# Performance work log

Hardware: AMD Instinct MI355X
Metric: run time of the kernel (lower is better)

The kernel has to match this reference:

```python
import jax, jax.numpy as jnp
import numpy as np

B, SV, SA, D, H, L, F = 1, 2048, 512, 1024, 16, 2, 4096
DH = D // H
S = SV + SA


def layer_norm(x):
    mu = jnp.mean(x, axis=-1, keepdims=True)
    var = jnp.var(x, axis=-1, keepdims=True)
    return (x - mu) * jax.lax.rsqrt(var + 1e-6)


def rms_norm(x, g):
    return x * jax.lax.rsqrt(jnp.mean(x * x, axis=-1, keepdims=True) + 1e-6) * g


def rope(x, theta):
    # x: [B,S,H*DH], theta: [S, DH//2] angles; complex-pair rotation as in rope_apply
    b, s, _ = x.shape
    x4 = x.reshape(b, s, H, DH)
    xe, xo = x4[..., 0::2], x4[..., 1::2]
    c = jnp.cos(theta)[None, :, None, :]
    sn = jnp.sin(theta)[None, :, None, :]
    re = xe * c - xo * sn
    im = xe * sn + xo * c
    return jnp.stack([re, im], axis=-1).reshape(b, s, H * DH)


def setup_inputs() -> dict:
    key = jax.random.key(0)
    ks = jax.random.split(key, 20)
    w = 0.02
    inp = {
        'video_tokens': jax.random.normal(ks[0], (B, SV, D), jnp.float32),
        'action_tokens': jax.random.normal(ks[1], (B, SA, D), jnp.float32),
        'video_freqs': jax.random.uniform(ks[2], (SV, DH // 2), jnp.float32) * 6.28,
        'action_freqs': jax.random.uniform(ks[3], (SA, DH // 2), jnp.float32) * 6.28,
        'video_t_mod': jax.random.normal(ks[4], (B, 6, D), jnp.float32),
        'action_t_mod': jax.random.normal(ks[5], (B, 6, D), jnp.float32),
        'Wq': jax.random.normal(ks[6], (2, L, D, D), jnp.float32) * w,
        'Wk': jax.random.normal(ks[7], (2, L, D, D), jnp.float32) * w,
        'Wv': jax.random.normal(ks[8], (2, L, D, D), jnp.float32) * w,
        'Wo': jax.random.normal(ks[9], (2, L, D, D), jnp.float32) * w,
        'bq': jnp.zeros((2, L, D), jnp.float32),
        'bk': jnp.zeros((2, L, D), jnp.float32),
        'bv': jnp.zeros((2, L, D), jnp.float32),
        'bo': jnp.zeros((2, L, D), jnp.float32),
        'gq': jnp.ones((2, L, D), jnp.float32),
        'gk': jnp.ones((2, L, D), jnp.float32),
        'mod': jax.random.normal(ks[10], (2, L, 6, D), jnp.float32) * 0.02,
        'W1': jax.random.normal(ks[11], (2, L, D, F), jnp.float32) * w,
        'b1': jnp.zeros((2, L, F), jnp.float32),
        'W2': jax.random.normal(ks[12], (2, L, F, D), jnp.float32) * w,
        'b2': jnp.zeros((2, L, D), jnp.float32),
    }
    # Mixed-modality ctx_mask: video bidirectional; action attends video + causal over action
    m = np.zeros((S, S), dtype=bool)
    m[:SV, :SV] = True
    m[SV:, :SV] = True
    m[SV:, SV:] = np.tril(np.ones((SA, SA), dtype=bool))
    inp['attention_mask'] = jnp.asarray(m)
    return inp


def _mot_forward(video_tokens, action_tokens, video_freqs, action_freqs,
                 video_t_mod, action_t_mod, Wq, Wk, Wv, Wo, bq, bk, bv, bo,
                 gq, gk, mod, W1, b1, W2, b2, attention_mask):
    xs = [video_tokens, action_tokens]
    thetas = [video_freqs, action_freqs]
    tmods = [video_t_mod, action_t_mod]
    scale = 1.0 / jnp.sqrt(jnp.asarray(DH, xs[0].dtype))
    for l in range(L):
        qs, kss, vs, posts = [], [], [], []
        for e in range(2):
            m6 = mod[e, l][None] + tmods[e]  # [B,6,D]
            sh_msa, sc_msa, g_msa, sh_mlp, sc_mlp, g_mlp = (
                m6[:, i:i + 1, :] for i in range(6))
            a = layer_norm(xs[e]) * (1.0 + sc_msa) + sh_msa
            q = rope(rms_norm(a @ Wq[e, l] + bq[e, l], gq[e, l]), thetas[e])
            k = rope(rms_norm(a @ Wk[e, l] + bk[e, l], gk[e, l]), thetas[e])
            v = a @ Wv[e, l] + bv[e, l]
            qs.append(q); kss.append(k); vs.append(v)
            posts.append((g_msa, sh_mlp, sc_mlp, g_mlp))
        qc = jnp.concatenate(qs, axis=1).reshape(B, S, H, DH)
        kc = jnp.concatenate(kss, axis=1).reshape(B, S, H, DH)
        vc = jnp.concatenate(vs, axis=1).reshape(B, S, H, DH)
        scores = jnp.einsum('bqhd,bkhd->bhqk', qc, kc) * scale
        scores = jnp.where(attention_mask[None, None], scores, -1e9)
        p = jax.nn.softmax(scores, axis=-1)
        o = jnp.einsum('bhqk,bkhd->bqhd', p, vc).reshape(B, S, H * DH)
        outs = [o[:, :SV], o[:, SV:]]
        for e in range(2):
            g_msa, sh_mlp, sc_mlp, g_mlp = posts[e]
            x = xs[e] + g_msa * (outs[e] @ Wo[e, l] + bo[e, l])
            mi = layer_norm(x) * (1.0 + sc_mlp) + sh_mlp
            h = jax.nn.gelu(mi @ W1[e, l] + b1[e, l], approximate=True) @ W2[e, l] + b2[e, l]
            xs[e] = x + g_mlp * h
    return jnp.concatenate(xs, axis=1)  # [B, SV+SA, D]


def reference(video_tokens, action_tokens, video_freqs, action_freqs,
              video_t_mod, action_t_mod, Wq, Wk, Wv, Wo, bq, bk, bv, bo,
              gq, gk, mod, W1, b1, W2, b2, attention_mask):
    return _mot_forward(video_tokens, action_tokens, video_freqs, action_freqs,
                        video_t_mod, action_t_mod, Wq, Wk, Wv, Wo, bq, bk, bv, bo,
                        gq, gk, mod, W1, b1, W2, b2, attention_mask)
```

## Files before the change

kernel.cpp:

```cpp
#include <hip/hip_runtime.h>
#include <hip/hip_bf16.h>

#define BF16 __hip_bfloat16
typedef short bf16x8 __attribute__((ext_vector_type(8)));
typedef float f32x4  __attribute__((ext_vector_type(4)));
typedef unsigned int u32;

#define MFMA16(a, b, c) __builtin_amdgcn_mfma_f32_16x16x32_bf16(a, b, c, 0, 0, 0)


__device__ __forceinline__ void async16(const void* g, void* l) {
  __builtin_amdgcn_global_load_lds(
      (const __attribute__((address_space(1))) u32*)g,
      (__attribute__((address_space(3))) u32*)l, 16, 0, 0);
}

__device__ __forceinline__ u32 pkbf(float a, float b) {
  union { BF16 h; unsigned short s; } ua, ub;
  ua.h = __float2bfloat16(a); ub.h = __float2bfloat16(b);
  return (u32)ua.s | ((u32)ub.s << 16);
}

__global__ __launch_bounds__(256) void wtrans(const float* __restrict__ W,
                                              BF16* __restrict__ WT, int K, int N,
                                              size_t outZ) {
  __shared__ float t[32][33];
  const float* Wm = W + (size_t)K * N * blockIdx.z;
  BF16* Tm = WT + outZ * blockIdx.z;
  int n0 = blockIdx.x * 32, k0 = blockIdx.y * 32;
  int tx = threadIdx.x & 31, ty = threadIdx.x >> 5;
#pragma unroll
  for (int i = 0; i < 4; i++)
    t[ty + 8 * i][tx] = Wm[(size_t)(k0 + ty + 8 * i) * N + n0 + tx];
  __syncthreads();
#pragma unroll
  for (int i = 0; i < 4; i++)
    Tm[(size_t)(n0 + ty + 8 * i) * K + k0 + tx] = __float2bfloat16(t[tx][ty + 8 * i]);
}

__global__ __launch_bounds__(256) void packb(const float* __restrict__ bq,
                                             const float* __restrict__ bk,
                                             const float* __restrict__ bv,
                                             float* __restrict__ bqkv) {
  int i = blockIdx.x * 256 + threadIdx.x;
  int s = i / 3072, c = i - s * 3072;
  float v = (c < 1024) ? bq[s * 1024 + c]
          : (c < 2048) ? bk[s * 1024 + c - 1024]
                       : bv[s * 1024 + c - 2048];
  bqkv[i] = v;
}

__global__ __launch_bounds__(256) void ln_mod(const float* __restrict__ x,
                                              BF16* __restrict__ out,
                                              const float* __restrict__ mod,
                                              const float* __restrict__ tmv,
                                              const float* __restrict__ tma,
                                              int l, int ish, int isc) {
  int r = blockIdx.x;
  int e = (r >= 2048) ? 1 : 0;
  const float* tm = e ? tma : tmv;
  const float* mo = mod + (size_t)((e * 2 + l) * 6) * 1024;
  float4 v = ((const float4*)(x + (size_t)r * 1024))[threadIdx.x];
  float s = v.x + v.y + v.z + v.w;
  float s2 = v.x * v.x + v.y * v.y + v.z * v.z + v.w * v.w;
#pragma unroll
  for (int off = 32; off >= 1; off >>= 1) {
    s += __shfl_down(s, off);
    s2 += __shfl_down(s2, off);
  }
  __shared__ float red[8];
  int lane = threadIdx.x & 63, w = threadIdx.x >> 6;
  if (lane == 0) { red[w] = s; red[4 + w] = s2; }
  __syncthreads();
  s = red[0] + red[1] + red[2] + red[3];
  s2 = red[4] + red[5] + red[6] + red[7];
  float mu = s * (1.f / 1024.f);
  float var = s2 * (1.f / 1024.f) - mu * mu;
  float inv = rsqrtf(var + 1e-6f);
  int c = threadIdx.x * 4;
  BF16* o = out + (size_t)r * 1024 + c;
  float xv[4] = {v.x, v.y, v.z, v.w};
#pragma unroll
  for (int k = 0; k < 4; k++) {
    float sc = mo[isc * 1024 + c + k] + tm[isc * 1024 + c + k];
    float sh = mo[ish * 1024 + c + k] + tm[ish * 1024 + c + k];
    o[k] = __float2bfloat16((xv[k] - mu) * inv * (1.f + sc) + sh);
  }
}

__global__ __launch_bounds__(256) void qk_post(const float* __restrict__ qkv,
                                               const float* __restrict__ gq,
                                               const float* __restrict__ gk,
                                               BF16* __restrict__ Qb, BF16* __restrict__ Kb,
                                               const float* __restrict__ vfreq,
                                               const float* __restrict__ afreq, int l) {
  int r = blockIdx.x;
  int which = blockIdx.y;
  const float* src = qkv + (size_t)r * 3072 + which * 1024;
  int e = (r >= 2048) ? 1 : 0;
  const float* g = (which ? gk : gq) + (size_t)(e * 2 + l) * 1024;
  BF16* dst = which ? Kb : Qb;
  const float* fr = e ? (afreq + (size_t)(r - 2048) * 32) : (vfreq + (size_t)r * 32);
  float4 v = ((const float4*)src)[threadIdx.x];
  float s2 = v.x * v.x + v.y * v.y + v.z * v.z + v.w * v.w;
#pragma unroll
  for (int off = 32; off >= 1; off >>= 1) s2 += __shfl_down(s2, off);
  __shared__ float red[4];
  int lane = threadIdx.x & 63, w = threadIdx.x >> 6;
  if (lane == 0) red[w] = s2;
  __syncthreads();
  s2 = red[0] + red[1] + red[2] + red[3];
  float inv = rsqrtf(s2 * (1.f / 1024.f) + 1e-6f);
  int c = threadIdx.x * 4;
  float xe0 = v.x * inv * g[c], xo0 = v.y * inv * g[c + 1];
  float xe1 = v.z * inv * g[c + 2], xo1 = v.w * inv * g[c + 3];
  int p0 = (c & 63) >> 1;
  float c0, s0, c1, s1;
  __sincosf(fr[p0], &s0, &c0);
  __sincosf(fr[p0 + 1], &s1, &c1);
  int h = c >> 6;
  size_t o = ((size_t)h * 2560 + r) * 64 + (c & 63);
  dst[o + 0] = __float2bfloat16(xe0 * c0 - xo0 * s0);
  dst[o + 1] = __float2bfloat16(xe0 * s0 + xo0 * c0);
  dst[o + 2] = __float2bfloat16(xe1 * c1 - xo1 * s1);
  dst[o + 3] = __float2bfloat16(xe1 * s1 + xo1 * c1);
}

__global__ __launch_bounds__(256) void vpost(const float* __restrict__ qkv,
                                             BF16* __restrict__ VT) {
  __shared__ float t[32][33];
  int r0 = blockIdx.x * 32, c0 = blockIdx.y * 32;
  int tx = threadIdx.x & 31, ty = threadIdx.x >> 5;
#pragma unroll
  for (int i = 0; i < 4; i++)
    t[ty + 8 * i][tx] = qkv[(size_t)(r0 + ty + 8 * i) * 3072 + 2048 + c0 + tx];
  __syncthreads();
#pragma unroll
  for (int i = 0; i < 4; i++)
    VT[(size_t)(c0 + ty + 8 * i) * 2560 + r0 + tx] = __float2bfloat16(t[tx][ty + 8 * i]);
}

template <int EPI, int KS>
__global__ __launch_bounds__(256) void gemm2(const BF16* __restrict__ A,
                                             const BF16* __restrict__ Bw, size_t Bestride,
                                             const float* __restrict__ bias, int biasE,
                                             void* __restrict__ out, float* __restrict__ part,
                                             int N, int K) {
  __shared__ BF16 As[128 * 64];
  __shared__ BF16 Bs[128 * 64];
  int flat = blockIdx.x + blockIdx.y * gridDim.x;
  int xcd = flat & 7, slot = flat >> 3;
  int bx = slot % gridDim.x;
  int by = (slot / gridDim.x) * 8 + xcd;
  int m0 = bx * 128, n0 = by * 128;
  int e = (m0 >= 2048);
  const BF16* Ab = A + (size_t)m0 * K;
  const BF16* Bb = Bw + (e ? Bestride : 0) + (size_t)n0 * K;
  int kz0 = blockIdx.z * (K / KS), kz1 = kz0 + K / KS;
  int tid = threadIdx.x, lane = tid & 63, w = tid >> 6;
  int wr = w & 1, wc = w >> 1;
  int m15 = lane & 15, q4 = lane >> 4;
  int L[4], rS[4], cS[4];
#pragma unroll
  for (int i = 0; i < 4; i++) {
    L[i] = w * 256 + i * 64 + lane;
    rS[i] = L[i] >> 3;
    cS[i] = (L[i] & 7) ^ (rS[i] & 7);
  }
  f32x4 acc[4][4] = {};
  for (int k0 = kz0; k0 < kz1; k0 += 64) {
    __syncthreads();
#pragma unroll
    for (int i = 0; i < 4; i++) {
      async16(Ab + (size_t)rS[i] * K + k0 + cS[i] * 8, &As[L[i] * 8]);
      async16(Bb + (size_t)rS[i] * K + k0 + cS[i] * 8, &Bs[L[i] * 8]);
    }
    __syncthreads();
#pragma unroll
    for (int kk = 0; kk < 2; kk++) {
      int pos = ((kk * 4 + q4) ^ (m15 & 7)) * 8;
      bf16x8 af[4], bv[4];
#pragma unroll
      for (int i = 0; i < 4; i++) af[i] = *(const bf16x8*)&As[(wr * 64 + i * 16 + m15) * 64 + pos];
#pragma unroll
      for (int j = 0; j < 4; j++) bv[j] = *(const bf16x8*)&Bs[(wc * 64 + j * 16 + m15) * 64 + pos];
#pragma unroll
      for (int i = 0; i < 4; i++)
#pragma unroll
        for (int j = 0; j < 4; j++)
          acc[i][j] = MFMA16(af[i], bv[j], acc[i][j]);
    }
  }
#pragma unroll
  for (int i = 0; i < 4; i++) {
    int row = m0 + wr * 64 + 16 * i + q4 * 4;
#pragma unroll
    for (int j = 0; j < 4; j++) {
      int col = n0 + wc * 64 + 16 * j + m15;
      float b = (EPI == 3) ? 0.f : bias[e * biasE + col];
#pragma unroll
      for (int rg = 0; rg < 4; rg++) {
        float v = acc[i][j][rg] + b;
        size_t idx = (size_t)(row + rg) * N + col;
        if (EPI == 0) {
          ((float*)out)[idx] = v;
        } else if (EPI == 1) {
          float u = 0.7978845608f * (v + 0.044715f * v * v * v);
          ((BF16*)out)[idx] = __float2bfloat16(0.5f * v * (1.f + tanhf(u)));
        } else {
          part[(size_t)blockIdx.z * 2560 * N + idx] = v;
        }
      }
    }
  }
}

template <int KS>
__global__ __launch_bounds__(256) void combine(const float* __restrict__ part,
                                               const float* __restrict__ biasL,
                                               const float* __restrict__ modp, int gi, int l,
                                               const float* __restrict__ tmv,
                                               const float* __restrict__ tma,
                                               const float* __restrict__ xin,
                                               float* __restrict__ xout) {
  int r = blockIdx.x, e = (r >= 2048) ? 1 : 0;
  int c = threadIdx.x * 4;
  float4 s = {0.f, 0.f, 0.f, 0.f};
#pragma unroll
  for (int z = 0; z < KS; z++) {
    float4 p = *(const float4*)&part[((size_t)z * 2560 + r) * 1024 + c];
    s.x += p.x; s.y += p.y; s.z += p.z; s.w += p.w;
  }
  float4 b = *(const float4*)&biasL[e * 2048 + c];
  const float* tm = e ? tma : tmv;
  float4 gm = *(const float4*)&modp[(size_t)((e * 2 + l) * 6 + gi) * 1024 + c];
  float4 gt = *(const float4*)&tm[gi * 1024 + c];
  float4 xi = *(const float4*)&xin[(size_t)r * 1024 + c];
  float4 o;
  o.x = xi.x + (gm.x + gt.x) * (s.x + b.x);
  o.y = xi.y + (gm.y + gt.y) * (s.y + b.y);
  o.z = xi.z + (gm.z + gt.z) * (s.z + b.z);
  o.w = xi.w + (gm.w + gt.w) * (s.w + b.w);
  *(float4*)&xout[(size_t)r * 1024 + c] = o;
}

__global__ __launch_bounds__(256) void flash2(const BF16* __restrict__ Qb,
                                              const BF16* __restrict__ Kb,
                                              const BF16* __restrict__ VT,
                                              BF16* __restrict__ O) {
  const int S = 2560;
  __shared__ BF16 Ks[2][128 * 64];
  __shared__ BF16 Vs[2][64 * 128];
  int tid = threadIdx.x, lane = tid & 63, w = tid >> 6;
  int h = blockIdx.y, q0 = blockIdx.x * 64;
  int m15 = lane & 15, q4 = lane >> 4;
  int actq = (q0 >= 2048);
  int nt = actq ? ((q0 + 64 + 127) >> 7) : 16;
  const BF16* qrow = Qb + ((size_t)h * S + q0 + w * 16 + m15) * 64;
  bf16x8 qf0 = *(const bf16x8*)(qrow + q4 * 8);
  bf16x8 qf1 = *(const bf16x8*)(qrow + 32 + q4 * 8);
  const BF16* kbase = Kb + (size_t)h * S * 64;
  const BF16* vbase = VT + (size_t)h * 64 * S;
  int Lk[4], rK[4], cK[4], rV[4], cV[4];
#pragma unroll
  for (int i = 0; i < 4; i++) {
    Lk[i] = w * 256 + i * 64 + lane;
    rK[i] = Lk[i] >> 3; cK[i] = (Lk[i] & 7) ^ (rK[i] & 7);
    rV[i] = Lk[i] >> 4; cV[i] = (Lk[i] & 15) ^ (rV[i] & 15);
  }
#pragma unroll
  for (int i = 0; i < 4; i++) {
    async16(kbase + (size_t)rK[i] * 64 + cK[i] * 8, &Ks[0][Lk[i] * 8]);
    async16(vbase + (size_t)rV[i] * S + cV[i] * 8, &Vs[0][Lk[i] * 8]);
  }
  f32x4 oa[4] = {};
  float m_i = -1e30f, l_i = 0.f;
  const float SC2 = 0.125f * 1.44269504f;
  int colq = q0 + w * 16 + m15;
  int sA = m15 + 16 * ((2 * q4) & 3);
  int sB = m15 + 16 * ((2 * q4 + 1) & 3);
  bool hi = (q4 >> 1) != 0;
  __syncthreads();
  for (int t = 0; t < nt; t++) {
    int cur = t & 1;
    if (t + 1 < nt) {
      int nb = cur ^ 1;
      const BF16* kg = kbase + (size_t)(t + 1) * 128 * 64;
      const BF16* vg = vbase + (size_t)(t + 1) * 128;
#pragma unroll
      for (int i = 0; i < 4; i++) {
        async16(kg + (size_t)rK[i] * 64 + cK[i] * 8, &Ks[nb][Lk[i] * 8]);
        async16(vg + (size_t)rV[i] * S + cV[i] * 8, &Vs[nb][Lk[i] * 8]);
      }
    }
    f32x4 st[8];
#pragma unroll
    for (int jt = 0; jt < 8; jt++) {
      int row = jt * 16 + m15;
      bf16x8 kf0 = *(const bf16x8*)&Ks[cur][row * 64 + ((q4 ^ (m15 & 7))) * 8];
      bf16x8 kf1 = *(const bf16x8*)&Ks[cur][row * 64 + (((4 + q4) ^ (m15 & 7))) * 8];
      f32x4 z = {};
      z = MFMA16(kf0, qf0, z);
      st[jt] = MFMA16(kf1, qf1, z);
    }
    float sv[8][4];
    float mx = -1e30f;
    bool dom = actq && (t == nt - 1);
#pragma unroll
    for (int jt = 0; jt < 8; jt++)
#pragma unroll
      for (int rg = 0; rg < 4; rg++) {
        float vv = st[jt][rg] * SC2;
        if (dom) {
          int rowkv = t * 128 + jt * 16 + q4 * 4 + rg;
          if (rowkv > colq) vv = -1e30f;
        }
        sv[jt][rg] = vv;
        mx = fmaxf(mx, vv);
      }
    mx = fmaxf(mx, __shfl_xor(mx, 16));
    mx = fmaxf(mx, __shfl_xor(mx, 32));
    float mn = fmaxf(m_i, mx);
    float al = exp2f(m_i - mn);
    m_i = mn;
    float rs = 0.f;
    u32 pk[16];
#pragma unroll
    for (int jt = 0; jt < 8; jt++) {
      float p0 = exp2f(sv[jt][0] - mn), p1 = exp2f(sv[jt][1] - mn);
      float p2 = exp2f(sv[jt][2] - mn), p3 = exp2f(sv[jt][3] - mn);
      rs += (p0 + p1) + (p2 + p3);
      pk[jt * 2 + 0] = pkbf(p0, p1);
      pk[jt * 2 + 1] = pkbf(p2, p3);
    }
    rs += __shfl_xor(rs, 16);
    rs += __shfl_xor(rs, 32);
    l_i = l_i * al + rs;
#pragma unroll
    for (int dt = 0; dt < 4; dt++)
#pragma unroll
      for (int rg = 0; rg < 4; rg++) oa[dt][rg] *= al;
#pragma unroll
    for (int kk = 0; kk < 4; kk++) {
      u32 a0 = __shfl((int)pk[4 * kk + 0], sA), c0_ = __shfl((int)pk[4 * kk + 2], sA);
      u32 a1 = __shfl((int)pk[4 * kk + 1], sA), c1_ = __shfl((int)pk[4 * kk + 3], sA);
      u32 b0 = __shfl((int)pk[4 * kk + 0], sB), d0 = __shfl((int)pk[4 * kk + 2], sB);
      u32 b1 = __shfl((int)pk[4 * kk + 1], sB), d1 = __shfl((int)pk[4 * kk + 3], sB);
      union { u32 u[4]; bf16x8 v; } pf;
      pf.u[0] = hi ? c0_ : a0;
      pf.u[1] = hi ? c1_ : a1;
      pf.u[2] = hi ? d0 : b0;
      pf.u[3] = hi ? d1 : b1;
#pragma unroll
      for (int dt = 0; dt < 4; dt++) {
        int vrow = dt * 16 + m15;
        bf16x8 vf = *(const bf16x8*)&Vs[cur][vrow * 128 + (((kk * 4 + q4) ^ m15)) * 8];
        oa[dt] = MFMA16(vf, pf.v, oa[dt]);
      }
    }
    __syncthreads();
  }
  float rl = 1.f / l_i;
  int orow = q0 + w * 16 + m15;
#pragma unroll
  for (int dt = 0; dt < 4; dt++) {
    int col = h * 64 + dt * 16 + q4 * 4;
    u32 lo = pkbf(oa[dt][0] * rl, oa[dt][1] * rl);
    u32 hi2 = pkbf(oa[dt][2] * rl, oa[dt][3] * rl);
    uint2 st2 = {lo, hi2};
    *(uint2*)&O[(size_t)orow * 1024 + col] = st2;
  }
}

extern "C" void kernel_launch(void* const* d_in, const int* in_sizes, int n_in,
                              void* d_out, int out_size, void* d_ws, size_t ws_size,
                              hipStream_t stream) {
  (void)in_sizes; (void)n_in; (void)out_size; (void)ws_size;
  const float* vid  = (const float*)d_in[0];
  const float* act  = (const float*)d_in[1];
  const float* vfr  = (const float*)d_in[2];
  const float* afr  = (const float*)d_in[3];
  const float* tmv  = (const float*)d_in[4];
  const float* tma  = (const float*)d_in[5];
  const float* Wq   = (const float*)d_in[6];
  const float* Wk   = (const float*)d_in[7];
  const float* Wv   = (const float*)d_in[8];
  const float* Wo   = (const float*)d_in[9];
  const float* bq   = (const float*)d_in[10];
  const float* bk   = (const float*)d_in[11];
  const float* bv   = (const float*)d_in[12];
  const float* bo   = (const float*)d_in[13];
  const float* gq   = (const float*)d_in[14];
  const float* gk   = (const float*)d_in[15];
  const float* modp = (const float*)d_in[16];
  const float* W1   = (const float*)d_in[17];
  const float* b1   = (const float*)d_in[18];
  const float* W2   = (const float*)d_in[19];
  const float* b2   = (const float*)d_in[20];

  char* p = (char*)d_ws;
  auto carve = [&](size_t bytes) {
    char* r = p;
    p += (bytes + 255) & ~(size_t)255;
    return r;
  };
  BF16* WqkvT = (BF16*)carve(4ull * 3072 * 1024 * 2);
  BF16* WoT   = (BF16*)carve(4ull * 1024 * 1024 * 2);
  BF16* W1T   = (BF16*)carve(4ull * 4096 * 1024 * 2);
  BF16* W2T   = (BF16*)carve(4ull * 1024 * 4096 * 2);
  float* bqkv = (float*)carve(4ull * 3072 * 4);
  float* x    = (float*)carve(2560ull * 1024 * 4);
  BF16* abf   = (BF16*)carve(2560ull * 1024 * 2);
  float* qkv  = (float*)carve(2560ull * 3072 * 4);
  BF16* Qb    = (BF16*)carve(2560ull * 1024 * 2);
  BF16* Kb    = (BF16*)carve(2560ull * 1024 * 2);
  float* part = qkv;
  BF16* VTb   = (BF16*)carve(2560ull * 1024 * 2);
  BF16* Obf   = (BF16*)carve(2560ull * 1024 * 2);
  BF16* mibf  = (BF16*)carve(2560ull * 1024 * 2);
  BF16* hbf   = (BF16*)carve(2560ull * 4096 * 2);

  hipMemcpyAsync(x, vid, 2048ull * 1024 * 4, hipMemcpyDeviceToDevice, stream);
  hipMemcpyAsync(x + 2048ull * 1024, act, 512ull * 1024 * 4, hipMemcpyDeviceToDevice, stream);

  const size_t S3 = 3072ull * 1024;
  wtrans<<<dim3(32, 32, 4), 256, 0, stream>>>(Wq, WqkvT, 1024, 1024, S3);
  wtrans<<<dim3(32, 32, 4), 256, 0, stream>>>(Wk, WqkvT + 1024ull * 1024, 1024, 1024, S3);
  wtrans<<<dim3(32, 32, 4), 256, 0, stream>>>(Wv, WqkvT + 2048ull * 1024, 1024, 1024, S3);
  wtrans<<<dim3(32, 32, 4), 256, 0, stream>>>(Wo, WoT, 1024, 1024, 1024ull * 1024);
  wtrans<<<dim3(128, 32, 4), 256, 0, stream>>>(W1, W1T, 1024, 4096, 4096ull * 1024);
  wtrans<<<dim3(32, 128, 4), 256, 0, stream>>>(W2, W2T, 4096, 1024, 1024ull * 4096);
  packb<<<48, 256, 0, stream>>>(bq, bk, bv, bqkv);

  for (int l = 0; l < 2; l++) {
    ln_mod<<<2560, 256, 0, stream>>>(x, abf, modp, tmv, tma, l, 0, 1);
    gemm2<0, 1><<<dim3(20, 24, 1), 256, 0, stream>>>(
        abf, WqkvT + (size_t)l * S3, 2 * S3, bqkv + l * 3072, 6144, qkv, nullptr, 3072, 1024);
    qk_post<<<dim3(2560, 2), 256, 0, stream>>>(qkv, gq, gk, Qb, Kb, vfr, afr, l);
    vpost<<<dim3(80, 32), 256, 0, stream>>>(qkv, VTb);
    flash2<<<dim3(40, 16), 256, 0, stream>>>(Qb, Kb, VTb, Obf);
    gemm2<3, 2><<<dim3(20, 8, 2), 256, 0, stream>>>(
        Obf, WoT + (size_t)l * 1024 * 1024, 2ull * 1024 * 1024, nullptr, 0, nullptr, part,
        1024, 1024);
    combine<2><<<2560, 256, 0, stream>>>(part, bo + l * 1024, modp, 2, l, tmv, tma, x, x);
    ln_mod<<<2560, 256, 0, stream>>>(x, mibf, modp, tmv, tma, l, 3, 4);
    gemm2<1, 1><<<dim3(20, 32, 1), 256, 0, stream>>>(
        mibf, W1T + (size_t)l * 4096 * 1024, 2ull * 4096 * 1024, b1 + l * 4096, 8192, hbf,
        nullptr, 4096, 1024);
    gemm2<3, 4><<<dim3(20, 8, 4), 256, 0, stream>>>(
        hbf, W2T + (size_t)l * 4096 * 1024, 2ull * 4096 * 1024, nullptr, 0, nullptr, part,
        1024, 4096);
    combine<4><<<2560, 256, 0, stream>>>(part, b2 + l * 1024, modp, 5, l, tmv, tma, x,
                                         (l == 1) ? (float*)d_out : x);
  }
}
```

Measured before the change: 818.1 us.

## Restructure flash attention with 64-key tiles and LDS-staged P

```diff
diff --git a/kernel.cpp b/kernel.cpp
--- a/kernel.cpp
+++ b/kernel.cpp
@@ -111,6 +111,7 @@
   __syncthreads();
   s2 = red[0] + red[1] + red[2] + red[3];
   float inv = rsqrtf(s2 * (1.f / 1024.f) + 1e-6f);
+  if (which == 0) inv *= 0.125f * 1.44269504f;
   int c = threadIdx.x * 4;
   float xe0 = v.x * inv * g[c], xo0 = v.y * inv * g[c + 1];
   float xe1 = v.z * inv * g[c + 2], xo1 = v.w * inv * g[c + 3];
@@ -244,132 +245,121 @@
   *(float4*)&xout[(size_t)r * 1024 + c] = o;
 }
 
-__global__ __launch_bounds__(256) void flash2(const BF16* __restrict__ Qb,
+__global__ __launch_bounds__(256) void flash3(const BF16* __restrict__ Qb,
                                               const BF16* __restrict__ Kb,
                                               const BF16* __restrict__ VT,
                                               BF16* __restrict__ O) {
   const int S = 2560;
-  __shared__ BF16 Ks[2][128 * 64];
-  __shared__ BF16 Vs[2][64 * 128];
+  __shared__ BF16 Ks[2][64 * 64];
+  __shared__ BF16 Vs[2][64 * 64];
+  __shared__ BF16 Ps[4][16 * 72];
   int tid = threadIdx.x, lane = tid & 63, w = tid >> 6;
   int h = blockIdx.y, q0 = blockIdx.x * 64;
   int m15 = lane & 15, q4 = lane >> 4;
   int actq = (q0 >= 2048);
-  int nt = actq ? ((q0 + 64 + 127) >> 7) : 16;
+  int nt = actq ? ((q0 >> 6) + 1) : 32;
   const BF16* qrow = Qb + ((size_t)h * S + q0 + w * 16 + m15) * 64;
   bf16x8 qf0 = *(const bf16x8*)(qrow + q4 * 8);
   bf16x8 qf1 = *(const bf16x8*)(qrow + 32 + q4 * 8);
   const BF16* kbase = Kb + (size_t)h * S * 64;
   const BF16* vbase = VT + (size_t)h * 64 * S;
-  int Lk[4], rK[4], cK[4], rV[4], cV[4];
-#pragma unroll
-  for (int i = 0; i < 4; i++) {
-    Lk[i] = w * 256 + i * 64 + lane;
-    rK[i] = Lk[i] >> 3; cK[i] = (Lk[i] & 7) ^ (rK[i] & 7);
-    rV[i] = Lk[i] >> 4; cV[i] = (Lk[i] & 15) ^ (rV[i] & 15);
-  }
-#pragma unroll
-  for (int i = 0; i < 4; i++) {
-    async16(kbase + (size_t)rK[i] * 64 + cK[i] * 8, &Ks[0][Lk[i] * 8]);
-    async16(vbase + (size_t)rV[i] * S + cV[i] * 8, &Vs[0][Lk[i] * 8]);
-  }
+  int L0 = w * 128 + lane, L1 = L0 + 64;
+  int r0 = L0 >> 3, c0 = (L0 & 7) ^ (r0 & 7);
+  int r1 = L1 >> 3, c1 = (L1 & 7) ^ (r1 & 7);
+  async16(kbase + (size_t)r0 * 64 + c0 * 8, &Ks[0][L0 * 8]);
+  async16(kbase + (size_t)r1 * 64 + c1 * 8, &Ks[0][L1 * 8]);
+  async16(vbase + (size_t)r0 * S + c0 * 8, &Vs[0][L0 * 8]);
+  async16(vbase + (size_t)r1 * S + c1 * 8, &Vs[0][L1 * 8]);
   f32x4 oa[4] = {};
   float m_i = -1e30f, l_i = 0.f;
-  const float SC2 = 0.125f * 1.44269504f;
   int colq = q0 + w * 16 + m15;
-  int sA = m15 + 16 * ((2 * q4) & 3);
-  int sB = m15 + 16 * ((2 * q4 + 1) & 3);
-  bool hi = (q4 >> 1) != 0;
+  BF16* Pw = &Ps[w][0];
+  int x0 = (q4 ^ (m15 & 7)) * 8, x1 = ((4 + q4) ^ (m15 & 7)) * 8;
   __syncthreads();
   for (int t = 0; t < nt; t++) {
     int cur = t & 1;
     if (t + 1 < nt) {
       int nb = cur ^ 1;
-      const BF16* kg = kbase + (size_t)(t + 1) * 128 * 64;
-      const BF16* vg = vbase + (size_t)(t + 1) * 128;
-#pragma unroll
-      for (int i = 0; i < 4; i++) {
-        async16(kg + (size_t)rK[i] * 64 + cK[i] * 8, &Ks[nb][Lk[i] * 8]);
-        async16(vg + (size_t)rV[i] * S + cV[i] * 8, &Vs[nb][Lk[i] * 8]);
-      }
-    }
-    f32x4 st[8];
-#pragma unroll
-    for (int jt = 0; jt < 8; jt++) {
-      int row = jt * 16 + m15;
-      bf16x8 kf0 = *(const bf16x8*)&Ks[cur][row * 64 + ((q4 ^ (m15 & 7))) * 8];
-      bf16x8 kf1 = *(const bf16x8*)&Ks[cur][row * 64 + (((4 + q4) ^ (m15 & 7))) * 8];
+      const BF16* kg = kbase + (size_t)(t + 1) * 64 * 64;
+      const BF16* vg = vbase + (size_t)(t + 1) * 64;
+      async16(kg + (size_t)r0 * 64 + c0 * 8, &Ks[nb][L0 * 8]);
+      async16(kg + (size_t)r1 * 64 + c1 * 8, &Ks[nb][L1 * 8]);
+      async16(vg + (size_t)r0 * S + c0 * 8, &Vs[nb][L0 * 8]);
+      async16(vg + (size_t)r1 * S + c1 * 8, &Vs[nb][L1 * 8]);
+    }
+    f32x4 st[4];
+#pragma unroll
+    for (int jt = 0; jt < 4; jt++) {
+      int row = (jt * 16 + m15) * 64;
+      bf16x8 kf0 = *(const bf16x8*)&Ks[cur][row + x0];
+      bf16x8 kf1 = *(const bf16x8*)&Ks[cur][row + x1];
       f32x4 z = {};
       z = MFMA16(kf0, qf0, z);
       st[jt] = MFMA16(kf1, qf1, z);
     }
-    float sv[8][4];
     float mx = -1e30f;
-    bool dom = actq && (t == nt - 1);
-#pragma unroll
-    for (int jt = 0; jt < 8; jt++)
-#pragma unroll
-      for (int rg = 0; rg < 4; rg++) {
-        float vv = st[jt][rg] * SC2;
-        if (dom) {
-          int rowkv = t * 128 + jt * 16 + q4 * 4 + rg;
-          if (rowkv > colq) vv = -1e30f;
+    if (actq && t == nt - 1) {
+#pragma unroll
+      for (int jt = 0; jt < 4; jt++)
+#pragma unroll
+        for (int rg = 0; rg < 4; rg++) {
+          int rowkv = t * 64 + jt * 16 + q4 * 4 + rg;
+          if (rowkv > colq) st[jt][rg] = -1e30f;
+          mx = fmaxf(mx, st[jt][rg]);
         }
-        sv[jt][rg] = vv;
-        mx = fmaxf(mx, vv);
-      }
+    } else {
+#pragma unroll
+      for (int jt = 0; jt < 4; jt++)
+        mx = fmaxf(fmaxf(fmaxf(mx, st[jt][0]), fmaxf(st[jt][1], st[jt][2])), st[jt][3]);
+    }
     mx = fmaxf(mx, __shfl_xor(mx, 16));
     mx = fmaxf(mx, __shfl_xor(mx, 32));
     float mn = fmaxf(m_i, mx);
     float al = exp2f(m_i - mn);
     m_i = mn;
     float rs = 0.f;
-    u32 pk[16];
-#pragma unroll
-    for (int jt = 0; jt < 8; jt++) {
-      float p0 = exp2f(sv[jt][0] - mn), p1 = exp2f(sv[jt][1] - mn);
-      float p2 = exp2f(sv[jt][2] - mn), p3 = exp2f(sv[jt][3] - mn);
+#pragma unroll
+    for (int jt = 0; jt < 4; jt++) {
+      float p0 = exp2f(st[jt][0] - mn), p1 = exp2f(st[jt][1] - mn);
+      float p2 = exp2f(st[jt][2] - mn), p3 = exp2f(st[jt][3] - mn);
       rs += (p0 + p1) + (p2 + p3);
-      pk[jt * 2 + 0] = pkbf(p0, p1);
-      pk[jt * 2 + 1] = pkbf(p2, p3);
+      uint2 pr = {pkbf(p0, p1), pkbf(p2, p3)};
+      *(uint2*)&Pw[m15 * 72 + jt * 16 + q4 * 4] = pr;
     }
     rs += __shfl_xor(rs, 16);
     rs += __shfl_xor(rs, 32);
     l_i = l_i * al + rs;
+    float alr[4];
+#pragma unroll
+    for (int rg = 0; rg < 4; rg++) alr[rg] = __shfl(al, q4 * 4 + rg);
 #pragma unroll
     for (int dt = 0; dt < 4; dt++)
 #pragma unroll
-      for (int rg = 0; rg < 4; rg++) oa[dt][rg] *= al;
-#pragma unroll
-    for (int kk = 0; kk < 4; kk++) {
-      u32 a0 = __shfl((int)pk[4 * kk + 0], sA), c0_ = __shfl((int)pk[4 * kk + 2], sA);
-      u32 a1 = __shfl((int)pk[4 * kk + 1], sA), c1_ = __shfl((int)pk[4 * kk + 3], sA);
-      u32 b0 = __shfl((int)pk[4 * kk + 0], sB), d0 = __shfl((int)pk[4 * kk + 2], sB);
-      u32 b1 = __shfl((int)pk[4 * kk + 1], sB), d1 = __shfl((int)pk[4 * kk + 3], sB);
-      union { u32 u[4]; bf16x8 v; } pf;
-      pf.u[0] = hi ? c0_ : a0;
-      pf.u[1] = hi ? c1_ : a1;
-      pf.u[2] = hi ? d0 : b0;
-      pf.u[3] = hi ? d1 : b1;
-#pragma unroll
-      for (int dt = 0; dt < 4; dt++) {
-        int vrow = dt * 16 + m15;
-        bf16x8 vf = *(const bf16x8*)&Vs[cur][vrow * 128 + (((kk * 4 + q4) ^ m15)) * 8];
-        oa[dt] = MFMA16(vf, pf.v, oa[dt]);
-      }
+      for (int rg = 0; rg < 4; rg++) oa[dt][rg] *= alr[rg];
+    bf16x8 pf0 = *(const bf16x8*)&Pw[m15 * 72 + q4 * 8];
+    bf16x8 pf1 = *(const bf16x8*)&Pw[m15 * 72 + 32 + q4 * 8];
+#pragma unroll
+    for (int dt = 0; dt < 4; dt++) {
+      int vr = (dt * 16 + m15) * 64;
+      bf16x8 vf0 = *(const bf16x8*)&Vs[cur][vr + x0];
+      bf16x8 vf1 = *(const bf16x8*)&Vs[cur][vr + x1];
+      oa[dt] = MFMA16(pf0, vf0, oa[dt]);
+      oa[dt] = MFMA16(pf1, vf1, oa[dt]);
     }
     __syncthreads();
   }
   float rl = 1.f / l_i;
-  int orow = q0 + w * 16 + m15;
-#pragma unroll
-  for (int dt = 0; dt < 4; dt++) {
-    int col = h * 64 + dt * 16 + q4 * 4;
-    u32 lo = pkbf(oa[dt][0] * rl, oa[dt][1] * rl);
-    u32 hi2 = pkbf(oa[dt][2] * rl, oa[dt][3] * rl);
-    uint2 st2 = {lo, hi2};
-    *(uint2*)&O[(size_t)orow * 1024 + col] = st2;
-  }
+  float rlr[4];
+#pragma unroll
+  for (int rg = 0; rg < 4; rg++) rlr[rg] = __shfl(rl, q4 * 4 + rg);
+#pragma unroll
+  for (int dt = 0; dt < 4; dt++)
+#pragma unroll
+    for (int rg = 0; rg < 4; rg++) {
+      int row = q0 + w * 16 + q4 * 4 + rg;
+      int col = h * 64 + dt * 16 + m15;
+      O[(size_t)row * 1024 + col] = __float2bfloat16(oa[dt][rg] * rlr[rg]);
+    }
 }
 
 extern "C" void kernel_launch(void* const* d_in, const int* in_sizes, int n_in,
@@ -438,7 +428,7 @@
         abf, WqkvT + (size_t)l * S3, 2 * S3, bqkv + l * 3072, 6144, qkv, nullptr, 3072, 1024);
     qk_post<<<dim3(2560, 2), 256, 0, stream>>>(qkv, gq, gk, Qb, Kb, vfr, afr, l);
     vpost<<<dim3(80, 32), 256, 0, stream>>>(qkv, VTb);
-    flash2<<<dim3(40, 16), 256, 0, stream>>>(Qb, Kb, VTb, Obf);
+    flash3<<<dim3(40, 16), 256, 0, stream>>>(Qb, Kb, VTb, Obf);
     gemm2<3, 2><<<dim3(20, 8, 2), 256, 0, stream>>>(
         Obf, WoT + (size_t)l * 1024 * 1024, 2ull * 1024 * 1024, nullptr, 0, nullptr, part,
         1024, 1024);
```

Result: faster. 781.9 us (-4.4%).
